# Optimization experiments

Measured on AMD Instinct MI355X. Metric: run time of the kernel, lower is better.

Reference implementation:

```python
import jax, jax.numpy as jnp
import numpy as np

B, N, H = 128, 2048, 128
FEAT = 15


def setup_inputs() -> dict:
    key = jax.random.key(0)
    ks = jax.random.split(key, 24)
    f32 = jnp.float32
    inp = {
        'x':   jax.random.normal(ks[0], (B, N), f32),
        'x1':  jax.random.uniform(ks[1], (B, N), f32),
        'x2':  jax.random.uniform(ks[2], (B, N), f32),
        'z1':  jax.random.uniform(ks[3], (B, N), f32),
        'z2':  jax.random.uniform(ks[4], (B, N), f32),
        'x1E': jax.random.uniform(ks[5], (B, N), f32),
        'x2E': jax.random.uniform(ks[6], (B, N), f32),
        'z1E': jax.random.uniform(ks[7], (B, N), f32),
        'z2E': jax.random.uniform(ks[8], (B, N), f32),
        'muB': jax.random.uniform(ks[9], (B, 1), f32, 0.01, 0.1),
        'lb':  jax.random.normal(ks[10], (B, N), f32) - 2.0,
        'ub':  jax.random.normal(ks[11], (B, N), f32) + 2.0,
        'has_lb': jnp.ones((B, N), bool),
        'has_ub': jnp.ones((B, N), bool),
        # LSTM params (PyTorch gate order i, f, g, o)
        'W_ih': 0.1 * jax.random.normal(ks[12], (4 * H, FEAT), f32),
        'W_hh': 0.1 * jax.random.normal(ks[13], (4 * H, H), f32),
        'b_ih': 0.1 * jax.random.normal(ks[14], (4 * H,), f32),
        'b_hh': 0.1 * jax.random.normal(ks[15], (4 * H,), f32),
        # px_head: Linear(H,H) -> ReLU -> Linear(H,1)
        'W1': 0.1 * jax.random.normal(ks[16], (H, H), f32),
        'b1': 0.1 * jax.random.normal(ks[17], (H,), f32),
        'W2': 0.1 * jax.random.normal(ks[18], (1, H), f32),
        'b2': 0.1 * jax.random.normal(ks[19], (1,), f32),
    }
    return inp


def _forward(x, x1, x2, z1, z2, x1E, x2E, z1E, z2E, muB, lb, ub,
             W_ih, W_hh, b_ih, b_hh, W1, b1, W2, b2, has_lb, has_ub):
    Bb, n = x.shape
    eps = 1e-12
    # slack / bad-coordinate handling
    z1 = jnp.where((z1 + muB) <= 0, 0.0, z1)
    z2 = jnp.where((z2 + muB) <= 0, 0.0, z2)
    # quadratic merit stand-in: M = 0.5(||x||^2 + ||z1||^2 + ||z2||^2)
    grad_x, grad_z1, grad_z2 = x, z1, z2
    invD1 = jnp.clip((z1 + muB) / (x1 + muB + eps), 0.0, 100.0)
    invD2 = jnp.clip((z2 + muB) / (x2 + muB + eps), 0.0, 100.0)
    muB_bn = jnp.broadcast_to(muB, (Bb, n))
    # [B, n, 15] -> [B*n, 15]
    feat = jnp.stack([x, x1, x2, z1, z2, grad_x, grad_z1, grad_z2,
                      x1E, x2E, z1E, z2E, muB_bn, invD1, invD2], axis=-1)
    feat = feat.reshape(Bb * n, FEAT)
    # single-step LSTM cell, h0 = c0 = 0 so W_hh @ h0 vanishes
    gates = feat @ W_ih.T + b_ih + b_hh          # [B*n, 4H]
    i, f, g, o = jnp.split(gates, 4, axis=-1)
    c = jax.nn.sigmoid(i) * jnp.tanh(g)
    h = jax.nn.sigmoid(o) * jnp.tanh(c)          # [B*n, H]
    # MLP head -> per-coordinate positive step size
    p = jax.nn.relu(h @ W1.T + b1) @ W2.T + b2   # [B*n, 1]
    p_x = jnp.abs(p).reshape(Bb, n)
    # elementwise updates
    d_x = -p_x * grad_x
    x_new = x + d_x
    z1 = z1 - invD1 * (-p_x * grad_x + grad_z1)
    z2 = z2 - invD2 * (p_x * grad_x + grad_z2)
    x = x_new  # project_step = identity accept
    x1 = jnp.where(has_lb, x - lb, 0.0)
    x2 = jnp.where(has_ub, ub - x, 0.0)
    return jnp.concatenate([x, x1, x2, z1, z2], axis=-1)  # [B, 5n]


def reference(x, x1, x2, z1, z2, x1E, x2E, z1E, z2E, muB, lb, ub,
              has_lb, has_ub, W_ih, W_hh, b_ih, b_hh, W1, b1, W2, b2):
    return _forward(x, x1, x2, z1, z2, x1E, x2E, z1E, z2E, muB, lb, ub,
                    W_ih, W_hh, b_ih, b_hh, W1, b1, W2, b2, has_lb, has_ub)
```

## Files before the change

kernel.cpp:

```cpp
#include <hip/hip_runtime.h>


typedef _Float16 half8v  __attribute__((ext_vector_type(8)));
typedef _Float16 half4v  __attribute__((ext_vector_type(4)));
typedef float    float4v __attribute__((ext_vector_type(4)));

#define N_SZ   2048
#define BLOCKT 1024
#define NWAVES 16
#define NBLK   512
#define WROWS  32

__device__ __forceinline__ float fast_rcp(float x) { return __builtin_amdgcn_rcpf(x); }
__device__ __forceinline__ float fast_exp2(float x) {
#if __has_builtin(__builtin_amdgcn_exp2f)
    return __builtin_amdgcn_exp2f(x);
#else
    return exp2f(x);
#endif
}

__device__ __forceinline__ half4v act4(float4v di, float4v dg, float4v dv) {
    half4v h;
    #pragma unroll
    for (int j = 0; j < 4; ++j) {
        const float u  = fast_exp2(di[j]);
        const float v  = fast_exp2(fminf(dg[j], 115.0f));
        const float w  = fast_exp2(fminf(dv[j], 115.0f));
        const float a3 = 1.0f + w;
        const float r  = fast_rcp((1.0f + u) * (1.0f + v) * a3);
        const float nm = (v - 1.0f) * r;
        const float cv = nm * a3;
        const float t  = cv * cv;
        const float P  = __builtin_fmaf(t, __builtin_fmaf(t, __builtin_fmaf(t,
                         -0.02714f, 0.12052f), -0.33157f), 0.99986f);
        h[j] = (_Float16)(nm * P);
    }
    return h;
}

__global__ __launch_bounds__(BLOCKT)
void ps_lstm_r15(const float* __restrict__ x_,
                 const float* __restrict__ x1_,
                 const float* __restrict__ x2_,
                 const float* __restrict__ z1_,
                 const float* __restrict__ z2_,
                 const float* __restrict__ x1E_,
                 const float* __restrict__ x2E_,
                 const float* __restrict__ z1E_,
                 const float* __restrict__ z2E_,
                 const float* __restrict__ muB_,
                 const float* __restrict__ lb_,
                 const float* __restrict__ ub_,
                 const float* __restrict__ Wih_,
                 const float* __restrict__ bih_,
                 const float* __restrict__ bhh_,
                 const float* __restrict__ W1_,
                 const float* __restrict__ b1_,
                 const float* __restrict__ W2_,
                 const float* __restrict__ b2_,
                 float* __restrict__ out_)
{
    __shared__ __align__(16) _Float16 fragWih[3 * 8 * 64 * 4];
    __shared__ __align__(16) _Float16 fragW1 [8 * 4 * 64 * 8];
    __shared__ __align__(16) _Float16 sFeat[NWAVES][WROWS * 16];
    __shared__ __align__(8)  float    sHead[2 * 128];

    const int tid  = threadIdx.x;
    const int lane = tid & 63;
    const int w    = tid >> 6;
    const int c    = lane & 15;
    const int q    = lane >> 4;

    for (int ch = tid; ch < 3 * 8 * 64; ch += BLOCKT) {
        const int g   = ch >> 9;
        const int rem = ch & 511;
        const int kk  = rem >> 6;
        const int l   = rem & 63;
        const int m   = kk * 16 + (l & 15);
        const int q4  = l >> 4;
        const int grow = (g == 0 ? m : (g == 1 ? 256 + m : 384 + m));
        const float gs = (g == 1) ? 2.8853901f : -1.4426950f;
        half4v hh;
        #pragma unroll
        for (int j = 0; j < 4; ++j) {
            const int k = q4 * 4 + j;
            const float raw = (k < 15) ? Wih_[grow * 15 + k]
                                       : (bih_[grow] + bhh_[grow]);
            hh[j] = (_Float16)(gs * raw);
        }
        *(half4v*)&fragWih[(size_t)ch * 4] = hh;
    }
    for (int ch = tid; ch < 8 * 4 * 64; ch += BLOCKT) {
        const int nt = ch >> 8;
        const int t  = (ch >> 6) & 3;
        const int l  = ch & 63;
        const int n2 = nt * 16 + (l & 15);
        const int q4 = l >> 4;
        const int k0 = 32 * t + q4 * 4;
        const int k1 = k0 + 16;
        const float4 a = *(const float4*)&W1_[n2 * 128 + k0];
        const float4 b = *(const float4*)&W1_[n2 * 128 + k1];
        half8v hh;
        hh[0] = (_Float16)a.x; hh[1] = (_Float16)a.y;
        hh[2] = (_Float16)a.z; hh[3] = (_Float16)a.w;
        hh[4] = (_Float16)b.x; hh[5] = (_Float16)b.y;
        hh[6] = (_Float16)b.z; hh[7] = (_Float16)b.w;
        *(half8v*)&fragW1[(size_t)ch * 8] = hh;
    }
    if (tid < 128) {
        sHead[2 * tid]     = b1_[tid];
        sHead[2 * tid + 1] = W2_[tid];
    }
    const float b2v = b2_[0];

    __syncthreads();

    const int rbase = (blockIdx.x * NWAVES + w) * WROWS;

    float ex = 0.f, ez1 = 0.f, ez2 = 0.f, eD1 = 0.f, eD2 = 0.f, elb = 0.f, eub = 0.f;
    if (lane < WROWS) {
        const int r = rbase + lane;
        const float x   = x_[r];
        const float x1  = x1_[r];
        const float x2  = x2_[r];
        float       z1  = z1_[r];
        float       z2  = z2_[r];
        const float x1E = x1E_[r];
        const float x2E = x2E_[r];
        const float z1E = z1E_[r];
        const float z2E = z2E_[r];
        const float mu  = muB_[r >> 11];

        z1 = ((z1 + mu) <= 0.0f) ? 0.0f : z1;
        z2 = ((z2 + mu) <= 0.0f) ? 0.0f : z2;
        float invD1 = (z1 + mu) * fast_rcp(x1 + mu + 1e-12f);
        float invD2 = (z2 + mu) * fast_rcp(x2 + mu + 1e-12f);
        invD1 = fminf(fmaxf(invD1, 0.0f), 100.0f);
        invD2 = fminf(fmaxf(invD2, 0.0f), 100.0f);

        const float f[15] = { x, x1, x2, z1, z2, x, z1, z2,
                              x1E, x2E, z1E, z2E, mu, invD1, invD2 };
        half8v f0, f1;
        #pragma unroll
        for (int k = 0; k < 8; ++k) f0[k] = (_Float16)f[k];
        #pragma unroll
        for (int k = 0; k < 7; ++k) f1[k] = (_Float16)f[8 + k];
        f1[7] = (_Float16)1.0f;
        *(half8v*)&sFeat[w][lane * 16]     = f0;
        *(half8v*)&sFeat[w][lane * 16 + 8] = f1;

        ex = x; ez1 = z1; ez2 = z2; eD1 = invD1; eD2 = invD2;
        elb = lb_[r]; eub = ub_[r];
    }

    const half4v fB0 = *(const half4v*)&sFeat[w][(c)      * 16 + q * 4];
    const half4v fB1 = *(const half4v*)&sFeat[w][(16 + c) * 16 + q * 4];

    half8v h0a, h1a, h2a, h3a, h0b, h1b, h2b, h3b;
#define GSTEP2(T, HA, HB) { \
    const _Float16* wp = fragWih + lane * 4 + (T) * 512; \
    const float4v zc = {0.f, 0.f, 0.f, 0.f}; \
    const half4v Ai0 = *(const half4v*)(wp); \
    const half4v Ag0 = *(const half4v*)(wp + 2048); \
    const half4v Ao0 = *(const half4v*)(wp + 4096); \
    const float4v diA0 = __builtin_amdgcn_mfma_f32_16x16x16f16(Ai0, fB0, zc, 0, 0, 0); \
    const float4v diB0 = __builtin_amdgcn_mfma_f32_16x16x16f16(Ai0, fB1, zc, 0, 0, 0); \
    const float4v dgA0 = __builtin_amdgcn_mfma_f32_16x16x16f16(Ag0, fB0, zc, 0, 0, 0); \
    const float4v dgB0 = __builtin_amdgcn_mfma_f32_16x16x16f16(Ag0, fB1, zc, 0, 0, 0); \
    const float4v dvA0 = __builtin_amdgcn_mfma_f32_16x16x16f16(Ao0, fB0, zc, 0, 0, 0); \
    const float4v dvB0 = __builtin_amdgcn_mfma_f32_16x16x16f16(Ao0, fB1, zc, 0, 0, 0); \
    const half4v hLoA = act4(diA0, dgA0, dvA0); \
    const half4v hLoB = act4(diB0, dgB0, dvB0); \
    const half4v Ai1 = *(const half4v*)(wp + 256); \
    const half4v Ag1 = *(const half4v*)(wp + 2048 + 256); \
    const half4v Ao1 = *(const half4v*)(wp + 4096 + 256); \
    const float4v diA1 = __builtin_amdgcn_mfma_f32_16x16x16f16(Ai1, fB0, zc, 0, 0, 0); \
    const float4v diB1 = __builtin_amdgcn_mfma_f32_16x16x16f16(Ai1, fB1, zc, 0, 0, 0); \
    const float4v dgA1 = __builtin_amdgcn_mfma_f32_16x16x16f16(Ag1, fB0, zc, 0, 0, 0); \
    const float4v dgB1 = __builtin_amdgcn_mfma_f32_16x16x16f16(Ag1, fB1, zc, 0, 0, 0); \
    const float4v dvA1 = __builtin_amdgcn_mfma_f32_16x16x16f16(Ao1, fB0, zc, 0, 0, 0); \
    const float4v dvB1 = __builtin_amdgcn_mfma_f32_16x16x16f16(Ao1, fB1, zc, 0, 0, 0); \
    const half4v hHiA = act4(diA1, dgA1, dvA1); \
    const half4v hHiB = act4(diB1, dgB1, dvB1); \
    HA[0] = hLoA[0]; HA[1] = hLoA[1]; HA[2] = hLoA[2]; HA[3] = hLoA[3]; \
    HA[4] = hHiA[0]; HA[5] = hHiA[1]; HA[6] = hHiA[2]; HA[7] = hHiA[3]; \
    HB[0] = hLoB[0]; HB[1] = hLoB[1]; HB[2] = hLoB[2]; HB[3] = hLoB[3]; \
    HB[4] = hHiB[0]; HB[5] = hHiB[1]; HB[6] = hHiB[2]; HB[7] = hHiB[3]; }
    GSTEP2(0, h0a, h0b)  GSTEP2(1, h1a, h1b)
    GSTEP2(2, h2a, h2b)  GSTEP2(3, h3a, h3b)
#undef GSTEP2

    float p0a = 0.f, p1a = 0.f, p2a = 0.f, p3a = 0.f;
    float p0b = 0.f, p1b = 0.f, p2b = 0.f, p3b = 0.f;
    #pragma unroll 1
    for (int nt = 0; nt < 8; ++nt) {
        const _Float16* w1p = fragW1 + lane * 8 + nt * 2048;
        const float4v zc = {0.f, 0.f, 0.f, 0.f};
        const half8v Bw0 = *(const half8v*)(w1p       );
        const half8v Bw1 = *(const half8v*)(w1p +  512);
        const half8v Bw2 = *(const half8v*)(w1p + 1024);
        const half8v Bw3 = *(const half8v*)(w1p + 1536);
        float4v accA, accB;
        accA = __builtin_amdgcn_mfma_f32_16x16x32_f16(h0a, Bw0, zc,   0, 0, 0);
        accB = __builtin_amdgcn_mfma_f32_16x16x32_f16(h0b, Bw0, zc,   0, 0, 0);
        accA = __builtin_amdgcn_mfma_f32_16x16x32_f16(h1a, Bw1, accA, 0, 0, 0);
        accB = __builtin_amdgcn_mfma_f32_16x16x32_f16(h1b, Bw1, accB, 0, 0, 0);
        accA = __builtin_amdgcn_mfma_f32_16x16x32_f16(h2a, Bw2, accA, 0, 0, 0);
        accB = __builtin_amdgcn_mfma_f32_16x16x32_f16(h2b, Bw2, accB, 0, 0, 0);
        accA = __builtin_amdgcn_mfma_f32_16x16x32_f16(h3a, Bw3, accA, 0, 0, 0);
        accB = __builtin_amdgcn_mfma_f32_16x16x32_f16(h3b, Bw3, accB, 0, 0, 0);
        const float2 bw = *(const float2*)(sHead + 2 * c + nt * 32);
        p0a = __builtin_fmaf(fmaxf(accA[0] + bw.x, 0.f), bw.y, p0a);
        p1a = __builtin_fmaf(fmaxf(accA[1] + bw.x, 0.f), bw.y, p1a);
        p2a = __builtin_fmaf(fmaxf(accA[2] + bw.x, 0.f), bw.y, p2a);
        p3a = __builtin_fmaf(fmaxf(accA[3] + bw.x, 0.f), bw.y, p3a);
        p0b = __builtin_fmaf(fmaxf(accB[0] + bw.x, 0.f), bw.y, p0b);
        p1b = __builtin_fmaf(fmaxf(accB[1] + bw.x, 0.f), bw.y, p1b);
        p2b = __builtin_fmaf(fmaxf(accB[2] + bw.x, 0.f), bw.y, p2b);
        p3b = __builtin_fmaf(fmaxf(accB[3] + bw.x, 0.f), bw.y, p3b);
    }

    #pragma unroll
    for (int s = 1; s <= 8; s <<= 1) {
        p0a += __shfl_xor(p0a, s, 64);
        p1a += __shfl_xor(p1a, s, 64);
        p2a += __shfl_xor(p2a, s, 64);
        p3a += __shfl_xor(p3a, s, 64);
        p0b += __shfl_xor(p0b, s, 64);
        p1b += __shfl_xor(p1b, s, 64);
        p2b += __shfl_xor(p2b, s, 64);
        p3b += __shfl_xor(p3b, s, 64);
    }
    const int srcl = ((lane >> 2) & 3) * 16;
    const float s0a = __shfl(p0a, srcl, 64);
    const float s1a = __shfl(p1a, srcl, 64);
    const float s2a = __shfl(p2a, srcl, 64);
    const float s3a = __shfl(p3a, srcl, 64);
    const float sAa = (lane & 1) ? s1a : s0a;
    const float sBa = (lane & 1) ? s3a : s2a;
    const float pr0 = (lane & 2) ? sBa : sAa;
    const float s0b = __shfl(p0b, srcl, 64);
    const float s1b = __shfl(p1b, srcl, 64);
    const float s2b = __shfl(p2b, srcl, 64);
    const float s3b = __shfl(p3b, srcl, 64);
    const float sAb = (lane & 1) ? s1b : s0b;
    const float sBb = (lane & 1) ? s3b : s2b;
    const float pr1 = (lane & 2) ? sBb : sAb;

    if (lane < WROWS) {
        const int   r     = rbase + lane;
        const int   b     = r >> 11;
        const int   n     = r & (N_SZ - 1);
        const float p     = ((lane < 16) ? pr0 : pr1) + b2v;
        const float pxx   = fabsf(p) * ex;
        const float x_new = ex - pxx;
        float* ob = out_ + (size_t)b * (5 * N_SZ) + n;
        ob[0 * N_SZ] = x_new;
        ob[1 * N_SZ] = x_new - elb;
        ob[2 * N_SZ] = eub - x_new;
        ob[3 * N_SZ] = ez1 - eD1 * (ez1 - pxx);
        ob[4 * N_SZ] = ez2 - eD2 * (ez2 + pxx);
    }
}

extern "C" void kernel_launch(void* const* d_in, const int* in_sizes, int n_in,
                              void* d_out, int out_size, void* d_ws, size_t ws_size,
                              hipStream_t stream) {
    (void)in_sizes; (void)n_in; (void)out_size; (void)d_ws; (void)ws_size;
    const float* x_   = (const float*)d_in[0];
    const float* x1_  = (const float*)d_in[1];
    const float* x2_  = (const float*)d_in[2];
    const float* z1_  = (const float*)d_in[3];
    const float* z2_  = (const float*)d_in[4];
    const float* x1E_ = (const float*)d_in[5];
    const float* x2E_ = (const float*)d_in[6];
    const float* z1E_ = (const float*)d_in[7];
    const float* z2E_ = (const float*)d_in[8];
    const float* muB_ = (const float*)d_in[9];
    const float* lb_  = (const float*)d_in[10];
    const float* ub_  = (const float*)d_in[11];
    const float* Wih_ = (const float*)d_in[14];
    const float* bih_ = (const float*)d_in[16];
    const float* bhh_ = (const float*)d_in[17];
    const float* W1_  = (const float*)d_in[18];
    const float* b1_  = (const float*)d_in[19];
    const float* W2_  = (const float*)d_in[20];
    const float* b2_  = (const float*)d_in[21];
    float* out_ = (float*)d_out;

    ps_lstm_r15<<<NBLK, BLOCKT, 0, stream>>>(
        x_, x1_, x2_, z1_, z2_, x1E_, x2E_, z1E_, z2E_, muB_, lb_, ub_,
        Wih_, bih_, bhh_, W1_, b1_, W2_, b2_, out_);
}
```

Baseline: 134.5 us.

## Process 64 rows per wave to double weight-fragment reuse and halve grid

Each wave now handles 64 rows instead of 32, so every lane loads and prepares one row and each loaded W_ih/W1 fragment feeds four MFMA row-tiles instead of two. The grid halves to 256 blocks, which halves the per-block cost of staging weights into shared memory and removes the idle half-wave in the elementwise prologue and epilogue. In exchange register pressure roughly doubles for the h fragments and accumulators, which may cause spills or lower occupancy. Fewer blocks also means less parallelism to spread across the CUs.

```diff
diff --git a/kernel.cpp b/kernel.cpp
--- a/kernel.cpp
+++ b/kernel.cpp
@@ -8,8 +8,8 @@
 #define N_SZ   2048
 #define BLOCKT 1024
 #define NWAVES 16
-#define NBLK   512
-#define WROWS  32
+#define NBLK   256
+#define WROWS  64
 
 __device__ __forceinline__ float fast_rcp(float x) { return __builtin_amdgcn_rcpf(x); }
 __device__ __forceinline__ float fast_exp2(float x) {
@@ -40,7 +40,7 @@
 }
 
 __global__ __launch_bounds__(BLOCKT)
-void ps_lstm_r15(const float* __restrict__ x_,
+void ps_lstm_r18(const float* __restrict__ x_,
                  const float* __restrict__ x1_,
                  const float* __restrict__ x2_,
                  const float* __restrict__ z1_,
@@ -118,9 +118,9 @@
 
     const int rbase = (blockIdx.x * NWAVES + w) * WROWS;
 
-    float ex = 0.f, ez1 = 0.f, ez2 = 0.f, eD1 = 0.f, eD2 = 0.f, elb = 0.f, eub = 0.f;
-    if (lane < WROWS) {
-        const int r = rbase + lane;
+    const int r = rbase + lane;
+    float ex, ez1, ez2, eD1, eD2, elb, eub;
+    {
         const float x   = x_[r];
         const float x1  = x1_[r];
         const float x2  = x2_[r];
@@ -156,9 +156,12 @@
 
     const half4v fB0 = *(const half4v*)&sFeat[w][(c)      * 16 + q * 4];
     const half4v fB1 = *(const half4v*)&sFeat[w][(16 + c) * 16 + q * 4];
+    const half4v fB2 = *(const half4v*)&sFeat[w][(32 + c) * 16 + q * 4];
+    const half4v fB3 = *(const half4v*)&sFeat[w][(48 + c) * 16 + q * 4];
 
     half8v h0a, h1a, h2a, h3a, h0b, h1b, h2b, h3b;
-#define GSTEP2(T, HA, HB) { \
+    half8v h0c, h1c, h2c, h3c, h0d, h1d, h2d, h3d;
+#define GSTEP4(T, HA, HB, HC, HD) { \
     const _Float16* wp = fragWih + lane * 4 + (T) * 512; \
     const float4v zc = {0.f, 0.f, 0.f, 0.f}; \
     const half4v Ai0 = *(const half4v*)(wp); \
@@ -166,33 +169,57 @@
     const half4v Ao0 = *(const half4v*)(wp + 4096); \
     const float4v diA0 = __builtin_amdgcn_mfma_f32_16x16x16f16(Ai0, fB0, zc, 0, 0, 0); \
     const float4v diB0 = __builtin_amdgcn_mfma_f32_16x16x16f16(Ai0, fB1, zc, 0, 0, 0); \
+    const float4v diC0 = __builtin_amdgcn_mfma_f32_16x16x16f16(Ai0, fB2, zc, 0, 0, 0); \
+    const float4v diD0 = __builtin_amdgcn_mfma_f32_16x16x16f16(Ai0, fB3, zc, 0, 0, 0); \
     const float4v dgA0 = __builtin_amdgcn_mfma_f32_16x16x16f16(Ag0, fB0, zc, 0, 0, 0); \
     const float4v dgB0 = __builtin_amdgcn_mfma_f32_16x16x16f16(Ag0, fB1, zc, 0, 0, 0); \
+    const float4v dgC0 = __builtin_amdgcn_mfma_f32_16x16x16f16(Ag0, fB2, zc, 0, 0, 0); \
+    const float4v dgD0 = __builtin_amdgcn_mfma_f32_16x16x16f16(Ag0, fB3, zc, 0, 0, 0); \
     const float4v dvA0 = __builtin_amdgcn_mfma_f32_16x16x16f16(Ao0, fB0, zc, 0, 0, 0); \
     const float4v dvB0 = __builtin_amdgcn_mfma_f32_16x16x16f16(Ao0, fB1, zc, 0, 0, 0); \
+    const float4v dvC0 = __builtin_amdgcn_mfma_f32_16x16x16f16(Ao0, fB2, zc, 0, 0, 0); \
+    const float4v dvD0 = __builtin_amdgcn_mfma_f32_16x16x16f16(Ao0, fB3, zc, 0, 0, 0); \
     const half4v hLoA = act4(diA0, dgA0, dvA0); \
     const half4v hLoB = act4(diB0, dgB0, dvB0); \
+    const half4v hLoC = act4(diC0, dgC0, dvC0); \
+    const half4v hLoD = act4(diD0, dgD0, dvD0); \
     const half4v Ai1 = *(const half4v*)(wp + 256); \
     const half4v Ag1 = *(const half4v*)(wp + 2048 + 256); \
     const half4v Ao1 = *(const half4v*)(wp + 4096 + 256); \
     const float4v diA1 = __builtin_amdgcn_mfma_f32_16x16x16f16(Ai1, fB0, zc, 0, 0, 0); \
     const float4v diB1 = __builtin_amdgcn_mfma_f32_16x16x16f16(Ai1, fB1, zc, 0, 0, 0); \
+    const float4v diC1 = __builtin_amdgcn_mfma_f32_16x16x16f16(Ai1, fB2, zc, 0, 0, 0); \
+    const float4v diD1 = __builtin_amdgcn_mfma_f32_16x16x16f16(Ai1, fB3, zc, 0, 0, 0); \
     const float4v dgA1 = __builtin_amdgcn_mfma_f32_16x16x16f16(Ag1, fB0, zc, 0, 0, 0); \
     const float4v dgB1 = __builtin_amdgcn_mfma_f32_16x16x16f16(Ag1, fB1, zc, 0, 0, 0); \
+    const float4v dgC1 = __builtin_amdgcn_mfma_f32_16x16x16f16(Ag1, fB2, zc, 0, 0, 0); \
+    const float4v dgD1 = __builtin_amdgcn_mfma_f32_16x16x16f16(Ag1, fB3, zc, 0, 0, 0); \
     const float4v dvA1 = __builtin_amdgcn_mfma_f32_16x16x16f16(Ao1, fB0, zc, 0, 0, 0); \
     const float4v dvB1 = __builtin_amdgcn_mfma_f32_16x16x16f16(Ao1, fB1, zc, 0, 0, 0); \
+    const float4v dvC1 = __builtin_amdgcn_mfma_f32_16x16x16f16(Ao1, fB2, zc, 0, 0, 0); \
+    const float4v dvD1 = __builtin_amdgcn_mfma_f32_16x16x16f16(Ao1, fB3, zc, 0, 0, 0); \
     const half4v hHiA = act4(diA1, dgA1, dvA1); \
     const half4v hHiB = act4(diB1, dgB1, dvB1); \
+    const half4v hHiC = act4(diC1, dgC1, dvC1); \
+    const half4v hHiD = act4(diD1, dgD1, dvD1); \
     HA[0] = hLoA[0]; HA[1] = hLoA[1]; HA[2] = hLoA[2]; HA[3] = hLoA[3]; \
     HA[4] = hHiA[0]; HA[5] = hHiA[1]; HA[6] = hHiA[2]; HA[7] = hHiA[3]; \
     HB[0] = hLoB[0]; HB[1] = hLoB[1]; HB[2] = hLoB[2]; HB[3] = hLoB[3]; \
-    HB[4] = hHiB[0]; HB[5] = hHiB[1]; HB[6] = hHiB[2]; HB[7] = hHiB[3]; }
-    GSTEP2(0, h0a, h0b)  GSTEP2(1, h1a, h1b)
-    GSTEP2(2, h2a, h2b)  GSTEP2(3, h3a, h3b)
-#undef GSTEP2
+    HB[4] = hHiB[0]; HB[5] = hHiB[1]; HB[6] = hHiB[2]; HB[7] = hHiB[3]; \
+    HC[0] = hLoC[0]; HC[1] = hLoC[1]; HC[2] = hLoC[2]; HC[3] = hLoC[3]; \
+    HC[4] = hHiC[0]; HC[5] = hHiC[1]; HC[6] = hHiC[2]; HC[7] = hHiC[3]; \
+    HD[0] = hLoD[0]; HD[1] = hLoD[1]; HD[2] = hLoD[2]; HD[3] = hLoD[3]; \
+    HD[4] = hHiD[0]; HD[5] = hHiD[1]; HD[6] = hHiD[2]; HD[7] = hHiD[3]; }
+    GSTEP4(0, h0a, h0b, h0c, h0d)
+    GSTEP4(1, h1a, h1b, h1c, h1d)
+    GSTEP4(2, h2a, h2b, h2c, h2d)
+    GSTEP4(3, h3a, h3b, h3c, h3d)
+#undef GSTEP4
 
     float p0a = 0.f, p1a = 0.f, p2a = 0.f, p3a = 0.f;
     float p0b = 0.f, p1b = 0.f, p2b = 0.f, p3b = 0.f;
+    float p0c = 0.f, p1c = 0.f, p2c = 0.f, p3c = 0.f;
+    float p0d = 0.f, p1d = 0.f, p2d = 0.f, p3d = 0.f;
     #pragma unroll 1
     for (int nt = 0; nt < 8; ++nt) {
         const _Float16* w1p = fragW1 + lane * 8 + nt * 2048;
@@ -201,15 +228,23 @@
         const half8v Bw1 = *(const half8v*)(w1p +  512);
         const half8v Bw2 = *(const half8v*)(w1p + 1024);
         const half8v Bw3 = *(const half8v*)(w1p + 1536);
-        float4v accA, accB;
+        float4v accA, accB, accC, accD;
         accA = __builtin_amdgcn_mfma_f32_16x16x32_f16(h0a, Bw0, zc,   0, 0, 0);
         accB = __builtin_amdgcn_mfma_f32_16x16x32_f16(h0b, Bw0, zc,   0, 0, 0);
+        accC = __builtin_amdgcn_mfma_f32_16x16x32_f16(h0c, Bw0, zc,   0, 0, 0);
+        accD = __builtin_amdgcn_mfma_f32_16x16x32_f16(h0d, Bw0, zc,   0, 0, 0);
         accA = __builtin_amdgcn_mfma_f32_16x16x32_f16(h1a, Bw1, accA, 0, 0, 0);
         accB = __builtin_amdgcn_mfma_f32_16x16x32_f16(h1b, Bw1, accB, 0, 0, 0);
+        accC = __builtin_amdgcn_mfma_f32_16x16x32_f16(h1c, Bw1, accC, 0, 0, 0);
+        accD = __builtin_amdgcn_mfma_f32_16x16x32_f16(h1d, Bw1, accD, 0, 0, 0);
         accA = __builtin_amdgcn_mfma_f32_16x16x32_f16(h2a, Bw2, accA, 0, 0, 0);
         accB = __builtin_amdgcn_mfma_f32_16x16x32_f16(h2b, Bw2, accB, 0, 0, 0);
+        accC = __builtin_amdgcn_mfma_f32_16x16x32_f16(h2c, Bw2, accC, 0, 0, 0);
+        accD = __builtin_amdgcn_mfma_f32_16x16x32_f16(h2d, Bw2, accD, 0, 0, 0);
         accA = __builtin_amdgcn_mfma_f32_16x16x32_f16(h3a, Bw3, accA, 0, 0, 0);
         accB = __builtin_amdgcn_mfma_f32_16x16x32_f16(h3b, Bw3, accB, 0, 0, 0);
+        accC = __builtin_amdgcn_mfma_f32_16x16x32_f16(h3c, Bw3, accC, 0, 0, 0);
+        accD = __builtin_amdgcn_mfma_f32_16x16x32_f16(h3d, Bw3, accD, 0, 0, 0);
         const float2 bw = *(const float2*)(sHead + 2 * c + nt * 32);
         p0a = __builtin_fmaf(fmaxf(accA[0] + bw.x, 0.f), bw.y, p0a);
         p1a = __builtin_fmaf(fmaxf(accA[1] + bw.x, 0.f), bw.y, p1a);
@@ -219,6 +254,14 @@
         p1b = __builtin_fmaf(fmaxf(accB[1] + bw.x, 0.f), bw.y, p1b);
         p2b = __builtin_fmaf(fmaxf(accB[2] + bw.x, 0.f), bw.y, p2b);
         p3b = __builtin_fmaf(fmaxf(accB[3] + bw.x, 0.f), bw.y, p3b);
+        p0c = __builtin_fmaf(fmaxf(accC[0] + bw.x, 0.f), bw.y, p0c);
+        p1c = __builtin_fmaf(fmaxf(accC[1] + bw.x, 0.f), bw.y, p1c);
+        p2c = __builtin_fmaf(fmaxf(accC[2] + bw.x, 0.f), bw.y, p2c);
+        p3c = __builtin_fmaf(fmaxf(accC[3] + bw.x, 0.f), bw.y, p3c);
+        p0d = __builtin_fmaf(fmaxf(accD[0] + bw.x, 0.f), bw.y, p0d);
+        p1d = __builtin_fmaf(fmaxf(accD[1] + bw.x, 0.f), bw.y, p1d);
+        p2d = __builtin_fmaf(fmaxf(accD[2] + bw.x, 0.f), bw.y, p2d);
+        p3d = __builtin_fmaf(fmaxf(accD[3] + bw.x, 0.f), bw.y, p3d);
     }
 
     #pragma unroll
@@ -231,28 +274,38 @@
         p1b += __shfl_xor(p1b, s, 64);
         p2b += __shfl_xor(p2b, s, 64);
         p3b += __shfl_xor(p3b, s, 64);
+        p0c += __shfl_xor(p0c, s, 64);
+        p1c += __shfl_xor(p1c, s, 64);
+        p2c += __shfl_xor(p2c, s, 64);
+        p3c += __shfl_xor(p3c, s, 64);
+        p0d += __shfl_xor(p0d, s, 64);
+        p1d += __shfl_xor(p1d, s, 64);
+        p2d += __shfl_xor(p2d, s, 64);
+        p3d += __shfl_xor(p3d, s, 64);
     }
     const int srcl = ((lane >> 2) & 3) * 16;
-    const float s0a = __shfl(p0a, srcl, 64);
-    const float s1a = __shfl(p1a, srcl, 64);
-    const float s2a = __shfl(p2a, srcl, 64);
-    const float s3a = __shfl(p3a, srcl, 64);
-    const float sAa = (lane & 1) ? s1a : s0a;
-    const float sBa = (lane & 1) ? s3a : s2a;
-    const float pr0 = (lane & 2) ? sBa : sAa;
-    const float s0b = __shfl(p0b, srcl, 64);
-    const float s1b = __shfl(p1b, srcl, 64);
-    const float s2b = __shfl(p2b, srcl, 64);
-    const float s3b = __shfl(p3b, srcl, 64);
-    const float sAb = (lane & 1) ? s1b : s0b;
-    const float sBb = (lane & 1) ? s3b : s2b;
-    const float pr1 = (lane & 2) ? sBb : sAb;
-
-    if (lane < WROWS) {
-        const int   r     = rbase + lane;
+#define ROUTE(P0, P1, P2, P3, PR) { \
+    const float s0v = __shfl(P0, srcl, 64); \
+    const float s1v = __shfl(P1, srcl, 64); \
+    const float s2v = __shfl(P2, srcl, 64); \
+    const float s3v = __shfl(P3, srcl, 64); \
+    const float sA  = (lane & 1) ? s1v : s0v; \
+    const float sB  = (lane & 1) ? s3v : s2v; \
+    PR = (lane & 2) ? sB : sA; }
+    float pr0, pr1, pr2, pr3;
+    ROUTE(p0a, p1a, p2a, p3a, pr0)
+    ROUTE(p0b, p1b, p2b, p3b, pr1)
+    ROUTE(p0c, p1c, p2c, p3c, pr2)
+    ROUTE(p0d, p1d, p2d, p3d, pr3)
+#undef ROUTE
+    const float sel01 = (lane & 16) ? pr1 : pr0;
+    const float sel23 = (lane & 16) ? pr3 : pr2;
+    const float prS   = (lane & 32) ? sel23 : sel01;
+
+    {
         const int   b     = r >> 11;
         const int   n     = r & (N_SZ - 1);
-        const float p     = ((lane < 16) ? pr0 : pr1) + b2v;
+        const float p     = prS + b2v;
         const float pxx   = fabsf(p) * ex;
         const float x_new = ex - pxx;
         float* ob = out_ + (size_t)b * (5 * N_SZ) + n;
@@ -289,7 +342,7 @@
     const float* b2_  = (const float*)d_in[21];
     float* out_ = (float*)d_out;
 
-    ps_lstm_r15<<<NBLK, BLOCKT, 0, stream>>>(
+    ps_lstm_r18<<<NBLK, BLOCKT, 0, stream>>>(
         x_, x1_, x2_, z1_, z2_, x1E_, x2E_, z1E_, z2E_, muB_, lb_, ub_,
         Wih_, bih_, bhh_, W1_, b1_, W2_, b2_, out_);
 }
```

After: 134.7 us. No clear change (+0.2%).
